# Kernel tuning notes

Hardware: AMD Instinct MI355X
Metric: run time of the kernel (lower is better)

The kernel has to match this reference:

```python
import jax, jax.numpy as jnp
import numpy as np

B, E, CIN, C, PRE, DME, DEN = 8, 64, 128, 128, 128, 32, 32
N_EDGE_TYPES, N_PATH_TYPES = 10, 20


def leaky(v):
    return jnp.where(v >= 0, v, 0.1 * v)


def setup_inputs() -> dict:
    key = jax.random.key(0)
    ks = jax.random.split(key, 30)
    s = 0.05
    inp = {
        'x': jax.random.normal(ks[0], (B, CIN, E), jnp.float32),
        'y': jax.random.normal(ks[1], (B, CIN, E), jnp.float32),
        'm_bias_mat': jax.random.normal(ks[2], (B, E, E), jnp.float32),
        'edge_mat': jax.random.randint(ks[3], (B, E, E), 0, N_EDGE_TYPES),
        'p_bias_mat': jax.random.normal(ks[4], (B, E, E, E), jnp.float32),
        'path_mat': jax.random.randint(ks[5], (B, E, E, E), 0, N_PATH_TYPES),
        'pre_out': jax.random.normal(ks[6], (B, PRE, E, E), jnp.float32),
        # parameters (conv1d/conv2d k=1 weights squeezed to matrices/vectors)
        'xc1_w': jax.random.normal(ks[7], (C, CIN), jnp.float32) * s,
        'yc1_w': jax.random.normal(ks[8], (C, CIN), jnp.float32) * s,
        'xc2_w': jax.random.normal(ks[9], (C,), jnp.float32) * s,
        'xc2_b': jax.random.normal(ks[10], (1,), jnp.float32) * s,
        'yc2_w': jax.random.normal(ks[11], (C,), jnp.float32) * s,
        'yc2_b': jax.random.normal(ks[12], (1,), jnp.float32) * s,
        'pconv_w': jax.random.normal(ks[13], (DEN,), jnp.float32) * s,
        'econv_w': jax.random.normal(ks[14], (DME,), jnp.float32) * s,
        'conv1_w': jax.random.normal(ks[15], (C, 2 * C + PRE), jnp.float32) * s,
        'conv1_b': jax.random.normal(ks[16], (C,), jnp.float32) * s,
        'conv2_w': jax.random.normal(ks[17], (C, C, 3, 3), jnp.float32) * s,
        'conv2_b': jax.random.normal(ks[18], (C,), jnp.float32) * s,
        'score_w': jax.random.normal(ks[19], (C,), jnp.float32) * s,
        'xlin_w': jax.random.normal(ks[20], (CIN, CIN), jnp.float32) * s,
        'ylin_w': jax.random.normal(ks[21], (CIN, CIN), jnp.float32) * s,
        'edge_table': jax.random.normal(ks[22], (N_EDGE_TYPES, DME), jnp.float32) * s,
        'path_table': jax.random.normal(ks[23], (N_PATH_TYPES, DEN), jnp.float32) * s,
    }
    return inp


def reference(x, y, m_bias_mat, edge_mat, p_bias_mat, path_mat, pre_out,
              xc1_w, yc1_w, xc2_w, xc2_b, yc2_w, yc2_b, pconv_w, econv_w,
              conv1_w, conv1_b, conv2_w, conv2_b, score_w, xlin_w, ylin_w,
              edge_table, path_table):
    # x,y: [B, CIN, E]; M == N == entity_num == E (required by path_fea reshape)
    x_f = jnp.einsum('ci,bim->bcm', xc1_w, x)                    # [B,C,M]
    y_f = jnp.einsum('ci,bin->bcn', yc1_w, y)                    # [B,C,N]
    x_self = jnp.einsum('c,bcm->bm', xc2_w, x_f) + xc2_b         # [B,M]
    y_other = jnp.einsum('c,bcn->bn', yc2_w, y_f) + yc2_b        # [B,N]
    # torch broadcast: [B,1,M] + [B,N,1] -> [B,N,M]
    logist = leaky(x_self[:, None, :] + y_other[:, :, None])     # [B,E,E]

    # ---- per-entity path attention (vectorized over entity axis e) ----
    path_embed = path_table[path_mat]                            # [B,E,M,N,DEN]
    path_logist = leaky(jnp.einsum('bemnd,d->bemn', path_embed, pconv_w))
    local = logist[:, None, :, :] + path_logist + p_bias_mat     # [B,E,M,N]
    A = jax.nn.softmax(local, axis=-1)
    x_ret = leaky(jnp.einsum('bemn,bcn->bcem', A, y_f) + x_f[:, :, None, :])  # [B,C,E,M]
    A2 = jax.nn.softmax(jnp.swapaxes(local, 2, 3), axis=-1)
    y_ret = leaky(jnp.einsum('benm,bcm->bcen', A2, x_f) + y_f[:, :, None, :])  # [B,C,E,N]
    path_fea = jnp.concatenate([x_ret, y_ret], axis=1)           # [B,2C,E,E]

    men = jnp.concatenate([path_fea, pre_out], axis=1)           # [B,2C+PRE,E,E]
    h = leaky(jnp.einsum('oc,bcij->boij', conv1_w, men) + conv1_b[None, :, None, None])
    h = jax.lax.conv_general_dilated(h, conv2_w, (1, 1), 'SAME',
                                     dimension_numbers=('NCHW', 'OIHW', 'NCHW'))
    men2rel = leaky(h + conv2_b[None, :, None, None])            # [B,C,E,E]

    scores = leaky(jnp.einsum('c,bcij->bij', score_w, men2rel))  # [B,E,E]
    edge_logist = leaky(jnp.einsum('bmnd,d->bmn', edge_table[edge_mat], econv_w))
    g = logist + scores + edge_logist + m_bias_mat               # [B,E,E]

    x_lin = jnp.einsum('ij,bjm->bmi', xlin_w, x)                 # [B,M,CIN]
    y_lin = jnp.einsum('ij,bjn->bni', ylin_w, y)                 # [B,N,CIN]
    G = jax.nn.softmax(g, axis=-1)
    out_x = jnp.einsum('bmn,bni->bim', G, y_lin) + x             # residual, [B,CIN,M]
    G2 = jax.nn.softmax(jnp.swapaxes(g, 1, 2), axis=-1)
    out_y = jnp.einsum('bnm,bmi->bin', G2, x_lin) + y            # [B,CIN,N]
    return (out_x, out_y, men2rel)
```

## Files before the change

kernel.cpp:

```cpp
#include <hip/hip_runtime.h>
#include <hip/hip_bf16.h>


typedef unsigned short u16;
typedef unsigned int u32;
typedef short s16x8 __attribute__((ext_vector_type(8)));
typedef float f32x4 __attribute__((ext_vector_type(4)));

#define NB 8
#define NE 64
#define NC 128

__device__ __forceinline__ float b2f(u16 u) { return __uint_as_float(((u32)u) << 16); }
__device__ __forceinline__ u16 f2b(float f) {
    u32 x = __float_as_uint(f);
    u32 r = (x + 0x7fffu + ((x >> 16) & 1u)) >> 16;
    return (u16)r;
}
__device__ __forceinline__ float lk(float v) { return v >= 0.f ? v : 0.1f * v; }
__device__ __forceinline__ s16x8 cvt8(const float* p) {
    float4 a = ((const float4*)p)[0], c = ((const float4*)p)[1];
    s16x8 r;
    r[0] = (short)f2b(a.x); r[1] = (short)f2b(a.y); r[2] = (short)f2b(a.z); r[3] = (short)f2b(a.w);
    r[4] = (short)f2b(c.x); r[5] = (short)f2b(c.y); r[6] = (short)f2b(c.z); r[7] = (short)f2b(c.w);
    return r;
}

__global__ __launch_bounds__(256) void k_prepw(const float* __restrict__ w1, const float* __restrict__ w2,
                                               u16* __restrict__ wA1, u16* __restrict__ wA2) {
    int idx = blockIdx.x * 256 + threadIdx.x;
    if (idx < 49152) {
        int e = idx & 7, lane = (idx >> 3) & 63, mtg = (idx >> 9) & 7, kc = idx >> 12;
        int o = mtg * 16 + (lane & 15), c = kc * 32 + ((lane >> 4) << 3) + e;
        wA1[idx] = f2b(w1[o * 384 + c]);
    } else {
        int id2 = idx - 49152;
        if (id2 < 147456) {
            int e = id2 & 7, lane = (id2 >> 3) & 63, mtg = (id2 >> 9) & 7;
            int kc = (id2 >> 12) & 3, tap = id2 >> 14;
            int o = mtg * 16 + (lane & 15), c = kc * 32 + ((lane >> 4) << 3) + e;
            wA2[id2] = f2b(w2[(o * 128 + c) * 9 + tap]);
        }
    }
}

__global__ __launch_bounds__(256) void k_front(const float* __restrict__ x, const float* __restrict__ y,
                                               const float* __restrict__ xc1, const float* __restrict__ yc1,
                                               const float* __restrict__ xc2w, const float* __restrict__ xc2b,
                                               const float* __restrict__ yc2w, const float* __restrict__ yc2b,
                                               const float* __restrict__ xlw, const float* __restrict__ ylw,
                                               const float* __restrict__ etab, const float* __restrict__ econv,
                                               const int* __restrict__ edge_mat, const float* __restrict__ m_bias,
                                               u16* __restrict__ xfb, u16* __restrict__ yfb,
                                               float* __restrict__ xfT, float* __restrict__ yfT,
                                               u16* __restrict__ xlT, u16* __restrict__ ylT,
                                               float* __restrict__ Lw, float* __restrict__ gb) {
    int b = blockIdx.x;
    int t = threadIdx.x;
    int lane = t & 63, w = t >> 6, l15 = lane & 15, q4 = lane >> 4;
    __shared__ u16 sxT[64][136];
    __shared__ u16 syT[64][136];
    __shared__ float sXs[64], sYo[64], sEd[16];

    if (t < 10) {
        float s = 0.f;
        for (int d = 0; d < 32; ++d) s += etab[t * 32 + d] * econv[d];
        sEd[t] = lk(s);
    }
    {
        int i = t >> 1, m0 = (t & 1) * 32;
        const float4* px = (const float4*)(x + (b * 128 + i) * 64 + m0);
        const float4* py = (const float4*)(y + (b * 128 + i) * 64 + m0);
#pragma unroll
        for (int q = 0; q < 8; ++q) {
            float4 v = px[q];
            int m = m0 + q * 4;
            sxT[m + 0][i] = f2b(v.x); sxT[m + 1][i] = f2b(v.y);
            sxT[m + 2][i] = f2b(v.z); sxT[m + 3][i] = f2b(v.w);
            float4 u = py[q];
            syT[m + 0][i] = f2b(u.x); syT[m + 1][i] = f2b(u.y);
            syT[m + 2][i] = f2b(u.z); syT[m + 3][i] = f2b(u.w);
        }
    }
    __syncthreads();

    int m = w * 16 + l15;

    {
        f32x4 acc[8];
#pragma unroll
        for (int mt = 0; mt < 8; ++mt) acc[mt] = (f32x4)(0.f);
#pragma unroll
        for (int kt = 0; kt < 4; ++kt) {
            s16x8 bfr = *(const s16x8*)&sxT[m][kt * 32 + q4 * 8];
#pragma unroll
            for (int mt = 0; mt < 8; ++mt) {
                s16x8 af = cvt8(xc1 + (mt * 16 + l15) * 128 + kt * 32 + q4 * 8);
                acc[mt] = __builtin_amdgcn_mfma_f32_16x16x32_bf16(af, bfr, acc[mt], 0, 0, 0);
            }
        }
        float xsp = 0.f;
#pragma unroll
        for (int mt = 0; mt < 8; ++mt) {
            int c0 = mt * 16 + q4 * 4;
            f32x4 a = acc[mt];
            xfb[(b * 128 + c0 + 0) * 64 + m] = f2b(a[0]);
            xfb[(b * 128 + c0 + 1) * 64 + m] = f2b(a[1]);
            xfb[(b * 128 + c0 + 2) * 64 + m] = f2b(a[2]);
            xfb[(b * 128 + c0 + 3) * 64 + m] = f2b(a[3]);
            *(float4*)(xfT + (b * 64 + m) * 128 + c0) = make_float4(a[0], a[1], a[2], a[3]);
            float4 wv = *(const float4*)(xc2w + c0);
            xsp += wv.x * a[0] + wv.y * a[1] + wv.z * a[2] + wv.w * a[3];
        }
        xsp += __shfl_xor(xsp, 16);
        xsp += __shfl_xor(xsp, 32);
        if (q4 == 0) sXs[m] = xsp + xc2b[0];
    }
    {
        f32x4 acc[8];
#pragma unroll
        for (int mt = 0; mt < 8; ++mt) acc[mt] = (f32x4)(0.f);
#pragma unroll
        for (int kt = 0; kt < 4; ++kt) {
            s16x8 bfr = *(const s16x8*)&syT[m][kt * 32 + q4 * 8];
#pragma unroll
            for (int mt = 0; mt < 8; ++mt) {
                s16x8 af = cvt8(yc1 + (mt * 16 + l15) * 128 + kt * 32 + q4 * 8);
                acc[mt] = __builtin_amdgcn_mfma_f32_16x16x32_bf16(af, bfr, acc[mt], 0, 0, 0);
            }
        }
        float ysp = 0.f;
#pragma unroll
        for (int mt = 0; mt < 8; ++mt) {
            int c0 = mt * 16 + q4 * 4;
            f32x4 a = acc[mt];
            yfb[(b * 128 + c0 + 0) * 64 + m] = f2b(a[0]);
            yfb[(b * 128 + c0 + 1) * 64 + m] = f2b(a[1]);
            yfb[(b * 128 + c0 + 2) * 64 + m] = f2b(a[2]);
            yfb[(b * 128 + c0 + 3) * 64 + m] = f2b(a[3]);
            *(float4*)(yfT + (b * 64 + m) * 128 + c0) = make_float4(a[0], a[1], a[2], a[3]);
            float4 wv = *(const float4*)(yc2w + c0);
            ysp += wv.x * a[0] + wv.y * a[1] + wv.z * a[2] + wv.w * a[3];
        }
        ysp += __shfl_xor(ysp, 16);
        ysp += __shfl_xor(ysp, 32);
        if (q4 == 0) sYo[m] = ysp + yc2b[0];
    }
    {
        f32x4 acc[8];
#pragma unroll
        for (int mt = 0; mt < 8; ++mt) acc[mt] = (f32x4)(0.f);
#pragma unroll
        for (int kt = 0; kt < 4; ++kt) {
            s16x8 bfr = *(const s16x8*)&sxT[m][kt * 32 + q4 * 8];
#pragma unroll
            for (int mt = 0; mt < 8; ++mt) {
                s16x8 af = cvt8(xlw + (mt * 16 + l15) * 128 + kt * 32 + q4 * 8);
                acc[mt] = __builtin_amdgcn_mfma_f32_16x16x32_bf16(af, bfr, acc[mt], 0, 0, 0);
            }
        }
#pragma unroll
        for (int mt = 0; mt < 8; ++mt) {
            int i0 = mt * 16 + q4 * 4;
            f32x4 a = acc[mt];
            xlT[(b * 128 + i0 + 0) * 64 + m] = f2b(a[0]);
            xlT[(b * 128 + i0 + 1) * 64 + m] = f2b(a[1]);
            xlT[(b * 128 + i0 + 2) * 64 + m] = f2b(a[2]);
            xlT[(b * 128 + i0 + 3) * 64 + m] = f2b(a[3]);
        }
    }
    {
        f32x4 acc[8];
#pragma unroll
        for (int mt = 0; mt < 8; ++mt) acc[mt] = (f32x4)(0.f);
#pragma unroll
        for (int kt = 0; kt < 4; ++kt) {
            s16x8 bfr = *(const s16x8*)&syT[m][kt * 32 + q4 * 8];
#pragma unroll
            for (int mt = 0; mt < 8; ++mt) {
                s16x8 af = cvt8(ylw + (mt * 16 + l15) * 128 + kt * 32 + q4 * 8);
                acc[mt] = __builtin_amdgcn_mfma_f32_16x16x32_bf16(af, bfr, acc[mt], 0, 0, 0);
            }
        }
#pragma unroll
        for (int mt = 0; mt < 8; ++mt) {
            int i0 = mt * 16 + q4 * 4;
            f32x4 a = acc[mt];
            ylT[(b * 128 + i0 + 0) * 64 + m] = f2b(a[0]);
            ylT[(b * 128 + i0 + 1) * 64 + m] = f2b(a[1]);
            ylT[(b * 128 + i0 + 2) * 64 + m] = f2b(a[2]);
            ylT[(b * 128 + i0 + 3) * 64 + m] = f2b(a[3]);
        }
    }
    __syncthreads();
#pragma unroll
    for (int r = 0; r < 16; ++r) {
        int idx = r * 256 + t;
        int i = idx >> 6, j = idx & 63;
        int gidx = b * 4096 + idx;
        float L = lk(sXs[j] + sYo[i]);
        Lw[gidx] = L;
        gb[gidx] = L + sEd[edge_mat[gidx]] + m_bias[gidx];
    }
}

__global__ __launch_bounds__(256) void k_attn(const float* __restrict__ Lw,
                                              const u16* __restrict__ xfb, const u16* __restrict__ yfb,
                                              const float* __restrict__ xfT, const float* __restrict__ yfT,
                                              const int* __restrict__ path_mat, const float* __restrict__ p_bias,
                                              const float* __restrict__ ptab, const float* __restrict__ pconv,
                                              const float* __restrict__ pre, u16* __restrict__ menT) {
    int b = blockIdx.x >> 6, e = blockIdx.x & 63;
    int t = threadIdx.x;
    int lane = t & 63, w = t >> 6;
    __shared__ float sA[64][68];
    __shared__ u16 Abf[64][72];
    __shared__ u16 E2bf[64][72];
    __shared__ float sRed[256];
    __shared__ float sPdot[20];

    if (t < 20) {
        float s = 0.f;
        for (int d = 0; d < 32; ++d) s += ptab[t * 32 + d] * pconv[d];
        sPdot[t] = lk(s);
    }
    __syncthreads();

    {
        int m = t >> 2, n0 = (t & 3) * 16;
        int base = (((b * 64 + e) * 64 + m) * 64 + n0);
        const int4* pm4 = (const int4*)(path_mat + base);
        const float4* pb4 = (const float4*)(p_bias + base);
        const float4* L4 = (const float4*)(Lw + (b * 64 + m) * 64 + n0);
#pragma unroll
        for (int q = 0; q < 4; ++q) {
            int4 pm = pm4[q]; float4 pb = pb4[q]; float4 l = L4[q];
            float4 v;
            v.x = l.x + sPdot[pm.x] + pb.x;
            v.y = l.y + sPdot[pm.y] + pb.y;
            v.z = l.z + sPdot[pm.z] + pb.z;
            v.w = l.w + sPdot[pm.w] + pb.w;
            *(float4*)&sA[m][n0 + q * 4] = v;
        }
    }
    __syncthreads();

    if (t < 128) {
        int r = t >> 1, h = t & 1;
        const float4* rp = (const float4*)&sA[r][h * 32];
        float mx = -1e30f;
#pragma unroll
        for (int k = 0; k < 8; ++k) {
            float4 v = rp[k];
            mx = fmaxf(mx, fmaxf(fmaxf(v.x, v.y), fmaxf(v.z, v.w)));
        }
        mx = fmaxf(mx, __shfl_xor(mx, 1));
        float s = 0.f;
#pragma unroll
        for (int k = 0; k < 8; ++k) {
            float4 v = rp[k];
            s += __expf(v.x - mx) + __expf(v.y - mx) + __expf(v.z - mx) + __expf(v.w - mx);
        }
        s += __shfl_xor(s, 1);
        if (h == 0) { sRed[r] = mx; sRed[64 + r] = 1.f / s; }
    } else {
        int n = (t - 128) >> 1, h = t & 1;
        float mx = -1e30f;
#pragma unroll
        for (int k = 0; k < 32; ++k) mx = fmaxf(mx, sA[h * 32 + k][n]);
        mx = fmaxf(mx, __shfl_xor(mx, 1));
        float s = 0.f;
#pragma unroll
        for (int k = 0; k < 32; ++k) s += __expf(sA[h * 32 + k][n] - mx);
        s += __shfl_xor(s, 1);
        if (h == 0) { sRed[128 + n] = mx; sRed[192 + n] = 1.f / s; }
    }
    __syncthreads();

    {
        int m = t >> 2, q = t & 3;
        float rmax = sRed[m], rinv = sRed[64 + m];
        const float4* rp = (const float4*)&sA[m][q * 16];
#pragma unroll
        for (int g2 = 0; g2 < 2; ++g2) {
            float4 v0 = rp[g2 * 2], v1 = rp[g2 * 2 + 1];
            s16x8 pk;
            pk[0] = (short)f2b(__expf(v0.x - rmax) * rinv);
            pk[1] = (short)f2b(__expf(v0.y - rmax) * rinv);
            pk[2] = (short)f2b(__expf(v0.z - rmax) * rinv);
            pk[3] = (short)f2b(__expf(v0.w - rmax) * rinv);
            pk[4] = (short)f2b(__expf(v1.x - rmax) * rinv);
            pk[5] = (short)f2b(__expf(v1.y - rmax) * rinv);
            pk[6] = (short)f2b(__expf(v1.z - rmax) * rinv);
            pk[7] = (short)f2b(__expf(v1.w - rmax) * rinv);
            *(s16x8*)&Abf[m][q * 16 + g2 * 8] = pk;
        }
    }
    {
        int n = t >> 2, q = t & 3;
        float cmax = sRed[128 + n], cinv = sRed[192 + n];
#pragma unroll
        for (int g2 = 0; g2 < 2; ++g2) {
            s16x8 pk;
#pragma unroll
            for (int k = 0; k < 8; ++k) {
                float v = sA[q * 16 + g2 * 8 + k][n];
                pk[k] = (short)f2b(__expf(v - cmax) * cinv);
            }
            *(s16x8*)&E2bf[n][q * 16 + g2 * 8] = pk;
        }
    }
    __syncthreads();

    int l15 = lane & 15, q4 = lane >> 4;
    {
        f32x4 acc[2][4];
#pragma unroll
        for (int ci = 0; ci < 2; ++ci)
#pragma unroll
            for (int mt = 0; mt < 4; ++mt) acc[ci][mt] = (f32x4)(0.f);
#pragma unroll
        for (int kt = 0; kt < 2; ++kt) {
            s16x8 afr[2];
#pragma unroll
            for (int ci = 0; ci < 2; ++ci) {
                int c = (2 * w + ci) * 16 + l15;
                afr[ci] = *(const s16x8*)(yfb + (b * 128 + c) * 64 + kt * 32 + q4 * 8);
            }
            s16x8 bfr[4];
#pragma unroll
            for (int mt = 0; mt < 4; ++mt)
                bfr[mt] = *(const s16x8*)&Abf[mt * 16 + l15][kt * 32 + q4 * 8];
#pragma unroll
            for (int ci = 0; ci < 2; ++ci)
#pragma unroll
                for (int mt = 0; mt < 4; ++mt)
                    acc[ci][mt] = __builtin_amdgcn_mfma_f32_16x16x32_bf16(afr[ci], bfr[mt], acc[ci][mt], 0, 0, 0);
        }
#pragma unroll
        for (int ci = 0; ci < 2; ++ci) {
            int c0 = (2 * w + ci) * 16 + q4 * 4;
#pragma unroll
            for (int mt = 0; mt < 4; ++mt) {
                int m = mt * 16 + l15;
                float4 res = *(const float4*)(xfT + (b * 64 + m) * 128 + c0);
                f32x4 a = acc[ci][mt];
                u32 lo = (u32)f2b(lk(a[0] + res.x)) | ((u32)f2b(lk(a[1] + res.y)) << 16);
                u32 hi = (u32)f2b(lk(a[2] + res.z)) | ((u32)f2b(lk(a[3] + res.w)) << 16);
                *(uint2*)(menT + ((b * 64 + e) * 64 + m) * 384 + c0) = make_uint2(lo, hi);
            }
        }
    }
    {
        f32x4 acc[2][4];
#pragma unroll
        for (int ci = 0; ci < 2; ++ci)
#pragma unroll
            for (int nt = 0; nt < 4; ++nt) acc[ci][nt] = (f32x4)(0.f);
#pragma unroll
        for (int kt = 0; kt < 2; ++kt) {
            s16x8 afr[2];
#pragma unroll
            for (int ci = 0; ci < 2; ++ci) {
                int c = (2 * w + ci) * 16 + l15;
                afr[ci] = *(const s16x8*)(xfb + (b * 128 + c) * 64 + kt * 32 + q4 * 8);
            }
            s16x8 bfr[4];
#pragma unroll
            for (int nt = 0; nt < 4; ++nt)
                bfr[nt] = *(const s16x8*)&E2bf[nt * 16 + l15][kt * 32 + q4 * 8];
#pragma unroll
            for (int ci = 0; ci < 2; ++ci)
#pragma unroll
                for (int nt = 0; nt < 4; ++nt)
                    acc[ci][nt] = __builtin_amdgcn_mfma_f32_16x16x32_bf16(afr[ci], bfr[nt], acc[ci][nt], 0, 0, 0);
        }
#pragma unroll
        for (int ci = 0; ci < 2; ++ci) {
            int c0 = (2 * w + ci) * 16 + q4 * 4;
#pragma unroll
            for (int nt = 0; nt < 4; ++nt) {
                int n = nt * 16 + l15;
                float4 res = *(const float4*)(yfT + (b * 64 + n) * 128 + c0);
                f32x4 a = acc[ci][nt];
                u32 lo = (u32)f2b(lk(a[0] + res.x)) | ((u32)f2b(lk(a[1] + res.y)) << 16);
                u32 hi = (u32)f2b(lk(a[2] + res.z)) | ((u32)f2b(lk(a[3] + res.w)) << 16);
                *(uint2*)(menT + ((b * 64 + e) * 64 + n) * 384 + 128 + c0) = make_uint2(lo, hi);
            }
        }
    }
    {
        int j = t & 63, pg = t >> 6;
#pragma unroll
        for (int oc = 0; oc < 4; ++oc) {
            int p0 = pg * 32 + oc * 8;
            s16x8 v;
#pragma unroll
            for (int k = 0; k < 8; ++k)
                v[k] = (short)f2b(pre[((b * 128 + p0 + k) * 64 + e) * 64 + j]);
            *(s16x8*)(menT + ((b * 64 + e) * 64 + j) * 384 + 256 + p0) = v;
        }
    }
}

__global__ __launch_bounds__(256) void k_conv1(const u16* __restrict__ menT, const u16* __restrict__ wA1,
                                               const float* __restrict__ b1, u16* __restrict__ hT) {
    int b = blockIdx.x >> 6, i = blockIdx.x & 63;
    int t = threadIdx.x;
    int lane = t & 63, w = t >> 6, wm = w & 1, wn = w >> 1;
    int l15 = lane & 15, q4 = lane >> 4;

    f32x4 acc[4][2];
#pragma unroll
    for (int mt = 0; mt < 4; ++mt)
#pragma unroll
        for (int nt = 0; nt < 2; ++nt) acc[mt][nt] = (f32x4)(0.f);

    const u16* mrow = menT + (b * 64 + i) * 64 * 384;
    for (int kc = 0; kc < 12; ++kc) {
        s16x8 af[4];
#pragma unroll
        for (int mt = 0; mt < 4; ++mt)
            af[mt] = *(const s16x8*)(wA1 + (((kc * 8 + wm * 4 + mt) * 64 + lane) << 3));
        s16x8 bf[2];
#pragma unroll
        for (int nt = 0; nt < 2; ++nt) {
            int j = (wn * 2 + nt) * 16 + l15;
            bf[nt] = *(const s16x8*)(mrow + j * 384 + kc * 32 + q4 * 8);
        }
#pragma unroll
        for (int mt = 0; mt < 4; ++mt)
#pragma unroll
            for (int nt = 0; nt < 2; ++nt)
                acc[mt][nt] = __builtin_amdgcn_mfma_f32_16x16x32_bf16(af[mt], bf[nt], acc[mt][nt], 0, 0, 0);
    }

#pragma unroll
    for (int mt = 0; mt < 4; ++mt) {
        int o0 = (wm * 4 + mt) * 16 + q4 * 4;
        float4 bb = *(const float4*)(b1 + o0);
#pragma unroll
        for (int nt = 0; nt < 2; ++nt) {
            int j = (wn * 2 + nt) * 16 + l15;
            f32x4 a = acc[mt][nt];
            u32 lo = (u32)f2b(lk(a[0] + bb.x)) | ((u32)f2b(lk(a[1] + bb.y)) << 16);
            u32 hi = (u32)f2b(lk(a[2] + bb.z)) | ((u32)f2b(lk(a[3] + bb.w)) << 16);
            *(uint2*)(hT + ((b * 64 + i) * 64 + j) * 128 + o0) = make_uint2(lo, hi);
        }
    }
}

__global__ __launch_bounds__(256) void k_conv2(const u16* __restrict__ hT, const u16* __restrict__ wA2,
                                               const float* __restrict__ b2, const float* __restrict__ score_w,
                                               const float* __restrict__ gb, float* __restrict__ m2r,
                                               float* __restrict__ g) {
    int b = blockIdx.x >> 6, i = blockIdx.x & 63;
    int t = threadIdx.x;
    int lane = t & 63, w = t >> 6, wm = w & 1, wn = w >> 1;
    int l15 = lane & 15, q4 = lane >> 4;
    __shared__ u16 sB2[3][66][136];
    __shared__ float sSc[2][64];

#pragma unroll
    for (int q = 0; q < 2; ++q) {
        int u = q * 256 + t;
        if (u < 384) {
            int r = u >> 7, rem = u & 127, hcol = rem >> 6, c2 = rem & 63;
            *(u32*)&sB2[r][hcol ? 65 : 0][c2 * 2] = 0u;
        }
    }
#pragma unroll
    for (int it = 0; it < 12; ++it) {
        int u = it * 256 + t;
        int cg = u & 15, j = (u >> 4) & 63, r = u >> 10;
        int ir = i - 1 + r;
        int4 v = make_int4(0, 0, 0, 0);
        if (ir >= 0 && ir < 64)
            v = *(const int4*)(hT + ((b * 64 + ir) * 64 + j) * 128 + cg * 8);
        *(int4*)&sB2[r][j + 1][cg * 8] = v;
    }
    __syncthreads();

    f32x4 acc[4][2];
#pragma unroll
    for (int mt = 0; mt < 4; ++mt)
#pragma unroll
        for (int nt = 0; nt < 2; ++nt) acc[mt][nt] = (f32x4)(0.f);

    for (int kc = 0; kc < 4; ++kc) {
#pragma unroll
        for (int tap = 0; tap < 9; ++tap) {
            int di = tap / 3, dj = tap % 3;
            s16x8 af[4];
#pragma unroll
            for (int mt = 0; mt < 4; ++mt)
                af[mt] = *(const s16x8*)(wA2 + ((((tap * 4 + kc) * 8 + wm * 4 + mt) * 64 + lane) << 3));
#pragma unroll
            for (int nt = 0; nt < 2; ++nt) {
                int jin = wn * 32 + nt * 16 + l15 + dj;
                s16x8 bf = *(const s16x8*)(&sB2[di][jin][kc * 32 + q4 * 8]);
#pragma unroll
                for (int mt = 0; mt < 4; ++mt)
                    acc[mt][nt] = __builtin_amdgcn_mfma_f32_16x16x32_bf16(af[mt], bf, acc[mt][nt], 0, 0, 0);
            }
        }
    }

    float part[2] = {0.f, 0.f};
#pragma unroll
    for (int mt = 0; mt < 4; ++mt) {
        int o0 = wm * 64 + mt * 16 + q4 * 4;
        float4 bb = *(const float4*)(b2 + o0);
        float4 sw = *(const float4*)(score_w + o0);
#pragma unroll
        for (int nt = 0; nt < 2; ++nt) {
            int j = wn * 32 + nt * 16 + l15;
            f32x4 a = acc[mt][nt];
            float v0 = lk(a[0] + bb.x), v1 = lk(a[1] + bb.y);
            float v2 = lk(a[2] + bb.z), v3 = lk(a[3] + bb.w);
            float* dst = m2r + ((b * 128 + o0) * 64 + i) * 64 + j;
            dst[0] = v0; dst[4096] = v1; dst[8192] = v2; dst[12288] = v3;
            part[nt] += sw.x * v0 + sw.y * v1 + sw.z * v2 + sw.w * v3;
        }
    }
#pragma unroll
    for (int nt = 0; nt < 2; ++nt) {
        float p = part[nt];
        p += __shfl_xor(p, 16);
        p += __shfl_xor(p, 32);
        if (q4 == 0) sSc[wm][wn * 32 + nt * 16 + l15] = p;
    }
    __syncthreads();
    if (t < 64) {
        float s = sSc[0][t] + sSc[1][t];
        int gi = (b * 64 + i) * 64 + t;
        g[gi] = gb[gi] + lk(s);
    }
}

__global__ __launch_bounds__(256) void k_gout(const float* __restrict__ g,
                                              const u16* __restrict__ xlT, const u16* __restrict__ ylT,
                                              const float* __restrict__ x, const float* __restrict__ y,
                                              float* __restrict__ out) {
    int b = blockIdx.x;
    int t = threadIdx.x;
    int lane = t & 63, w = t >> 6, l15 = lane & 15, q4 = lane >> 4;
    __shared__ float sG[64][68];
    __shared__ u16 Gbf[64][72];
    __shared__ u16 G2bf[64][72];
    __shared__ float sRed[256];

#pragma unroll
    for (int r = 0; r < 16; ++r) {
        int idx = r * 256 + t;
        sG[idx >> 6][idx & 63] = g[b * 4096 + idx];
    }
    __syncthreads();

    if (t < 128) {
        int r = t >> 1, h = t & 1;
        const float4* rp = (const float4*)&sG[r][h * 32];
        float mx = -1e30f;
#pragma unroll
        for (int k = 0; k < 8; ++k) {
            float4 v = rp[k];
            mx = fmaxf(mx, fmaxf(fmaxf(v.x, v.y), fmaxf(v.z, v.w)));
        }
        mx = fmaxf(mx, __shfl_xor(mx, 1));
        float s = 0.f;
#pragma unroll
        for (int k = 0; k < 8; ++k) {
            float4 v = rp[k];
            s += __expf(v.x - mx) + __expf(v.y - mx) + __expf(v.z - mx) + __expf(v.w - mx);
        }
        s += __shfl_xor(s, 1);
        if (h == 0) { sRed[r] = mx; sRed[64 + r] = 1.f / s; }
    } else {
        int n = (t - 128) >> 1, h = t & 1;
        float mx = -1e30f;
#pragma unroll
        for (int k = 0; k < 32; ++k) mx = fmaxf(mx, sG[h * 32 + k][n]);
        mx = fmaxf(mx, __shfl_xor(mx, 1));
        float s = 0.f;
#pragma unroll
        for (int k = 0; k < 32; ++k) s += __expf(sG[h * 32 + k][n] - mx);
        s += __shfl_xor(s, 1);
        if (h == 0) { sRed[128 + n] = mx; sRed[192 + n] = 1.f / s; }
    }
    __syncthreads();

    {
        int m = t >> 2, q = t & 3;
        float rmax = sRed[m], rinv = sRed[64 + m];
        const float4* rp = (const float4*)&sG[m][q * 16];
#pragma unroll
        for (int g2 = 0; g2 < 2; ++g2) {
            float4 v0 = rp[g2 * 2], v1 = rp[g2 * 2 + 1];
            s16x8 pk;
            pk[0] = (short)f2b(__expf(v0.x - rmax) * rinv);
            pk[1] = (short)f2b(__expf(v0.y - rmax) * rinv);
            pk[2] = (short)f2b(__expf(v0.z - rmax) * rinv);
            pk[3] = (short)f2b(__expf(v0.w - rmax) * rinv);
            pk[4] = (short)f2b(__expf(v1.x - rmax) * rinv);
            pk[5] = (short)f2b(__expf(v1.y - rmax) * rinv);
            pk[6] = (short)f2b(__expf(v1.z - rmax) * rinv);
            pk[7] = (short)f2b(__expf(v1.w - rmax) * rinv);
            *(s16x8*)&Gbf[m][q * 16 + g2 * 8] = pk;
        }
    }
    {
        int n = t >> 2, q = t & 3;
        float cmax = sRed[128 + n], cinv = sRed[192 + n];
#pragma unroll
        for (int g2 = 0; g2 < 2; ++g2) {
            s16x8 pk;
#pragma unroll
            for (int k = 0; k < 8; ++k) {
                float v = sG[q * 16 + g2 * 8 + k][n];
                pk[k] = (short)f2b(__expf(v - cmax) * cinv);
            }
            *(s16x8*)&G2bf[n][q * 16 + g2 * 8] = pk;
        }
    }
    __syncthreads();

    int mcol = w * 16 + l15;
    {
        f32x4 acc[8];
#pragma unroll
        for (int mt = 0; mt < 8; ++mt) acc[mt] = (f32x4)(0.f);
#pragma unroll
        for (int kt = 0; kt < 2; ++kt) {
            s16x8 bfr = *(const s16x8*)&Gbf[mcol][kt * 32 + q4 * 8];
#pragma unroll
            for (int mt = 0; mt < 8; ++mt) {
                s16x8 af = *(const s16x8*)(ylT + (b * 128 + mt * 16 + l15) * 64 + kt * 32 + q4 * 8);
                acc[mt] = __builtin_amdgcn_mfma_f32_16x16x32_bf16(af, bfr, acc[mt], 0, 0, 0);
            }
        }
#pragma unroll
        for (int mt = 0; mt < 8; ++mt) {
            int i0 = mt * 16 + q4 * 4;
            f32x4 a = acc[mt];
#pragma unroll
            for (int r = 0; r < 4; ++r) {
                int ad = (b * 128 + i0 + r) * 64 + mcol;
                out[ad] = a[r] + x[ad];
            }
        }
    }
    {
        f32x4 acc[8];
#pragma unroll
        for (int mt = 0; mt < 8; ++mt) acc[mt] = (f32x4)(0.f);
#pragma unroll
        for (int kt = 0; kt < 2; ++kt) {
            s16x8 bfr = *(const s16x8*)&G2bf[mcol][kt * 32 + q4 * 8];
#pragma unroll
            for (int mt = 0; mt < 8; ++mt) {
                s16x8 af = *(const s16x8*)(xlT + (b * 128 + mt * 16 + l15) * 64 + kt * 32 + q4 * 8);
                acc[mt] = __builtin_amdgcn_mfma_f32_16x16x32_bf16(af, bfr, acc[mt], 0, 0, 0);
            }
        }
#pragma unroll
        for (int mt = 0; mt < 8; ++mt) {
            int i0 = mt * 16 + q4 * 4;
            f32x4 a = acc[mt];
#pragma unroll
            for (int r = 0; r < 4; ++r) {
                int ad = (b * 128 + i0 + r) * 64 + mcol;
                out[65536 + ad] = a[r] + y[ad];
            }
        }
    }
}

extern "C" void kernel_launch(void* const* d_in, const int* in_sizes, int n_in,
                              void* d_out, int out_size, void* d_ws, size_t ws_size,
                              hipStream_t stream) {
    const float* x = (const float*)d_in[0];
    const float* y = (const float*)d_in[1];
    const float* m_bias = (const float*)d_in[2];
    const int* edge_mat = (const int*)d_in[3];
    const float* p_bias = (const float*)d_in[4];
    const int* path_mat = (const int*)d_in[5];
    const float* pre = (const float*)d_in[6];
    const float* xc1 = (const float*)d_in[7];
    const float* yc1 = (const float*)d_in[8];
    const float* xc2w = (const float*)d_in[9];
    const float* xc2b = (const float*)d_in[10];
    const float* yc2w = (const float*)d_in[11];
    const float* yc2b = (const float*)d_in[12];
    const float* pconv = (const float*)d_in[13];
    const float* econv = (const float*)d_in[14];
    const float* w1 = (const float*)d_in[15];
    const float* b1 = (const float*)d_in[16];
    const float* w2 = (const float*)d_in[17];
    const float* b2 = (const float*)d_in[18];
    const float* score_w = (const float*)d_in[19];
    const float* xlw = (const float*)d_in[20];
    const float* ylw = (const float*)d_in[21];
    const float* etab = (const float*)d_in[22];
    const float* ptab = (const float*)d_in[23];

    float* Lw = (float*)d_ws;
    float* gb = Lw + 32768;
    float* g = gb + 32768;
    float* xfT = g + 32768;
    float* yfT = xfT + 65536;
    u16* wA1 = (u16*)(yfT + 65536);
    u16* wA2 = wA1 + 49152;
    u16* xfb = wA2 + 147456;
    u16* yfb = xfb + 65536;
    u16* xlT = yfb + 65536;
    u16* ylT = xlT + 65536;
    u16* menT = ylT + 65536;
    u16* hT = menT + 12582912;

    float* out = (float*)d_out;
    float* out_m2r = out + 131072;

    hipLaunchKernelGGL(k_prepw, dim3(768), dim3(256), 0, stream, w1, w2, wA1, wA2);
    hipLaunchKernelGGL(k_front, dim3(8), dim3(256), 0, stream, x, y, xc1, yc1, xc2w, xc2b,
                       yc2w, yc2b, xlw, ylw, etab, econv, edge_mat, m_bias,
                       xfb, yfb, xfT, yfT, xlT, ylT, Lw, gb);
    hipLaunchKernelGGL(k_attn, dim3(512), dim3(256), 0, stream, Lw, xfb, yfb, xfT, yfT,
                       path_mat, p_bias, ptab, pconv, pre, menT);
    hipLaunchKernelGGL(k_conv1, dim3(512), dim3(256), 0, stream, menT, wA1, b1, hT);
    hipLaunchKernelGGL(k_conv2, dim3(512), dim3(256), 0, stream, hT, wA2, b2, score_w, gb,
                       out_m2r, g);
    hipLaunchKernelGGL(k_gout, dim3(8), dim3(256), 0, stream, g, xlT, ylT, x, y, out);
}
```

Measured before the change: 219.0 us.

## Merge weight prep and front projections into one wide kernel, split gout by direction

The weight-reformat kernel and the 8-block front kernel are combined into a single launch. The four projection GEMMs now run in separate blocks (32 instead of 8), and the pre_out-to-menT transpose moves out of k_attn into extra blocks of the same launch. The leaky logit matrix and the gb buffer are no longer stored; they are recomputed from per-node Xs/Yo vectors inside k_attn and k_conv2. The output kernel splits the row and column softmax paths across twice as many blocks. The aim is to remove a serial low-parallelism stage and a launch, at the cost of some recomputation and a larger mixed-role grid.

```diff
diff --git a/kernel.cpp b/kernel.cpp
--- a/kernel.cpp
+++ b/kernel.cpp
@@ -6,10 +6,6 @@
 typedef unsigned int u32;
 typedef short s16x8 __attribute__((ext_vector_type(8)));
 typedef float f32x4 __attribute__((ext_vector_type(4)));
-
-#define NB 8
-#define NE 64
-#define NC 128
 
 __device__ __forceinline__ float b2f(u16 u) { return __uint_as_float(((u32)u) << 16); }
 __device__ __forceinline__ u16 f2b(float f) {
@@ -26,190 +22,127 @@
     return r;
 }
 
-__global__ __launch_bounds__(256) void k_prepw(const float* __restrict__ w1, const float* __restrict__ w2,
-                                               u16* __restrict__ wA1, u16* __restrict__ wA2) {
-    int idx = blockIdx.x * 256 + threadIdx.x;
-    if (idx < 49152) {
-        int e = idx & 7, lane = (idx >> 3) & 63, mtg = (idx >> 9) & 7, kc = idx >> 12;
-        int o = mtg * 16 + (lane & 15), c = kc * 32 + ((lane >> 4) << 3) + e;
-        wA1[idx] = f2b(w1[o * 384 + c]);
-    } else {
-        int id2 = idx - 49152;
-        if (id2 < 147456) {
-            int e = id2 & 7, lane = (id2 >> 3) & 63, mtg = (id2 >> 9) & 7;
-            int kc = (id2 >> 12) & 3, tap = id2 >> 14;
+__global__ __launch_bounds__(256) void k_prep(const float* __restrict__ w1, const float* __restrict__ w2,
+                                              u16* __restrict__ wA1, u16* __restrict__ wA2,
+                                              const float* __restrict__ x, const float* __restrict__ y,
+                                              const float* __restrict__ xc1, const float* __restrict__ yc1,
+                                              const float* __restrict__ xc2w, const float* __restrict__ xc2b,
+                                              const float* __restrict__ yc2w, const float* __restrict__ yc2b,
+                                              const float* __restrict__ xlw, const float* __restrict__ ylw,
+                                              u16* __restrict__ xfb, u16* __restrict__ yfb,
+                                              float* __restrict__ xfT, float* __restrict__ yfT,
+                                              u16* __restrict__ xlT, u16* __restrict__ ylT,
+                                              float* __restrict__ Xs, float* __restrict__ Yo,
+                                              const float* __restrict__ pre, u16* __restrict__ menT) {
+    int bid = blockIdx.x;
+    int t = threadIdx.x;
+    if (bid < 768) {
+        int idx = bid * 256 + t;
+        if (idx < 49152) {
+            int e = idx & 7, lane = (idx >> 3) & 63, mtg = (idx >> 9) & 7, kc = idx >> 12;
             int o = mtg * 16 + (lane & 15), c = kc * 32 + ((lane >> 4) << 3) + e;
-            wA2[id2] = f2b(w2[(o * 128 + c) * 9 + tap]);
-        }
-    }
-}
-
-__global__ __launch_bounds__(256) void k_front(const float* __restrict__ x, const float* __restrict__ y,
-                                               const float* __restrict__ xc1, const float* __restrict__ yc1,
-                                               const float* __restrict__ xc2w, const float* __restrict__ xc2b,
-                                               const float* __restrict__ yc2w, const float* __restrict__ yc2b,
-                                               const float* __restrict__ xlw, const float* __restrict__ ylw,
-                                               const float* __restrict__ etab, const float* __restrict__ econv,
-                                               const int* __restrict__ edge_mat, const float* __restrict__ m_bias,
-                                               u16* __restrict__ xfb, u16* __restrict__ yfb,
-                                               float* __restrict__ xfT, float* __restrict__ yfT,
-                                               u16* __restrict__ xlT, u16* __restrict__ ylT,
-                                               float* __restrict__ Lw, float* __restrict__ gb) {
-    int b = blockIdx.x;
-    int t = threadIdx.x;
-    int lane = t & 63, w = t >> 6, l15 = lane & 15, q4 = lane >> 4;
-    __shared__ u16 sxT[64][136];
-    __shared__ u16 syT[64][136];
-    __shared__ float sXs[64], sYo[64], sEd[16];
-
-    if (t < 10) {
-        float s = 0.f;
-        for (int d = 0; d < 32; ++d) s += etab[t * 32 + d] * econv[d];
-        sEd[t] = lk(s);
+            wA1[idx] = f2b(w1[o * 384 + c]);
+        } else {
+            int id2 = idx - 49152;
+            if (id2 < 147456) {
+                int e = id2 & 7, lane = (id2 >> 3) & 63, mtg = (id2 >> 9) & 7;
+                int kc = (id2 >> 12) & 3, tap = id2 >> 14;
+                int o = mtg * 16 + (lane & 15), c = kc * 32 + ((lane >> 4) << 3) + e;
+                wA2[id2] = f2b(w2[(o * 128 + c) * 9 + tap]);
+            }
+        }
+        return;
+    }
+    if (bid < 800) {
+        int r = bid - 768;
+        int b = r >> 2, g4 = r & 3;
+        int lane = t & 63, w = t >> 6, l15 = lane & 15, q4 = lane >> 4;
+        __shared__ u16 sT[64][136];
+        const float* src = (g4 == 0 || g4 == 2) ? x : y;
+        const float* wptr = (g4 == 0) ? xc1 : (g4 == 1) ? yc1 : (g4 == 2) ? xlw : ylw;
+        {
+            int i = t >> 1, m0 = (t & 1) * 32;
+            const float4* ps = (const float4*)(src + (b * 128 + i) * 64 + m0);
+#pragma unroll
+            for (int q = 0; q < 8; ++q) {
+                float4 v = ps[q];
+                int m = m0 + q * 4;
+                sT[m + 0][i] = f2b(v.x); sT[m + 1][i] = f2b(v.y);
+                sT[m + 2][i] = f2b(v.z); sT[m + 3][i] = f2b(v.w);
+            }
+        }
+        __syncthreads();
+        int m = w * 16 + l15;
+        f32x4 acc[8];
+#pragma unroll
+        for (int mt = 0; mt < 8; ++mt) acc[mt] = (f32x4)(0.f);
+#pragma unroll
+        for (int kt = 0; kt < 4; ++kt) {
+            s16x8 bfr = *(const s16x8*)&sT[m][kt * 32 + q4 * 8];
+#pragma unroll
+            for (int mt = 0; mt < 8; ++mt) {
+                s16x8 af = cvt8(wptr + (mt * 16 + l15) * 128 + kt * 32 + q4 * 8);
+                acc[mt] = __builtin_amdgcn_mfma_f32_16x16x32_bf16(af, bfr, acc[mt], 0, 0, 0);
+            }
+        }
+        if (g4 == 0 || g4 == 1) {
+            u16* fb = (g4 == 0) ? xfb : yfb;
+            float* fT = (g4 == 0) ? xfT : yfT;
+            const float* c2w = (g4 == 0) ? xc2w : yc2w;
+            const float* c2b = (g4 == 0) ? xc2b : yc2b;
+            float* dvec = (g4 == 0) ? Xs : Yo;
+            float sp = 0.f;
+#pragma unroll
+            for (int mt = 0; mt < 8; ++mt) {
+                int c0 = mt * 16 + q4 * 4;
+                f32x4 a = acc[mt];
+                fb[(b * 128 + c0 + 0) * 64 + m] = f2b(a[0]);
+                fb[(b * 128 + c0 + 1) * 64 + m] = f2b(a[1]);
+                fb[(b * 128 + c0 + 2) * 64 + m] = f2b(a[2]);
+                fb[(b * 128 + c0 + 3) * 64 + m] = f2b(a[3]);
+                *(float4*)(fT + (b * 64 + m) * 128 + c0) = make_float4(a[0], a[1], a[2], a[3]);
+                float4 wv = *(const float4*)(c2w + c0);
+                sp += wv.x * a[0] + wv.y * a[1] + wv.z * a[2] + wv.w * a[3];
+            }
+            sp += __shfl_xor(sp, 16);
+            sp += __shfl_xor(sp, 32);
+            if (q4 == 0) dvec[b * 64 + m] = sp + c2b[0];
+        } else {
+            u16* lT = (g4 == 2) ? xlT : ylT;
+#pragma unroll
+            for (int mt = 0; mt < 8; ++mt) {
+                int i0 = mt * 16 + q4 * 4;
+                f32x4 a = acc[mt];
+                lT[(b * 128 + i0 + 0) * 64 + m] = f2b(a[0]);
+                lT[(b * 128 + i0 + 1) * 64 + m] = f2b(a[1]);
+                lT[(b * 128 + i0 + 2) * 64 + m] = f2b(a[2]);
+                lT[(b * 128 + i0 + 3) * 64 + m] = f2b(a[3]);
+            }
+        }
+        return;
     }
     {
-        int i = t >> 1, m0 = (t & 1) * 32;
-        const float4* px = (const float4*)(x + (b * 128 + i) * 64 + m0);
-        const float4* py = (const float4*)(y + (b * 128 + i) * 64 + m0);
-#pragma unroll
-        for (int q = 0; q < 8; ++q) {
-            float4 v = px[q];
-            int m = m0 + q * 4;
-            sxT[m + 0][i] = f2b(v.x); sxT[m + 1][i] = f2b(v.y);
-            sxT[m + 2][i] = f2b(v.z); sxT[m + 3][i] = f2b(v.w);
-            float4 u = py[q];
-            syT[m + 0][i] = f2b(u.x); syT[m + 1][i] = f2b(u.y);
-            syT[m + 2][i] = f2b(u.z); syT[m + 3][i] = f2b(u.w);
-        }
-    }
-    __syncthreads();
-
-    int m = w * 16 + l15;
-
-    {
-        f32x4 acc[8];
-#pragma unroll
-        for (int mt = 0; mt < 8; ++mt) acc[mt] = (f32x4)(0.f);
-#pragma unroll
-        for (int kt = 0; kt < 4; ++kt) {
-            s16x8 bfr = *(const s16x8*)&sxT[m][kt * 32 + q4 * 8];
-#pragma unroll
-            for (int mt = 0; mt < 8; ++mt) {
-                s16x8 af = cvt8(xc1 + (mt * 16 + l15) * 128 + kt * 32 + q4 * 8);
-                acc[mt] = __builtin_amdgcn_mfma_f32_16x16x32_bf16(af, bfr, acc[mt], 0, 0, 0);
-            }
-        }
-        float xsp = 0.f;
-#pragma unroll
-        for (int mt = 0; mt < 8; ++mt) {
-            int c0 = mt * 16 + q4 * 4;
-            f32x4 a = acc[mt];
-            xfb[(b * 128 + c0 + 0) * 64 + m] = f2b(a[0]);
-            xfb[(b * 128 + c0 + 1) * 64 + m] = f2b(a[1]);
-            xfb[(b * 128 + c0 + 2) * 64 + m] = f2b(a[2]);
-            xfb[(b * 128 + c0 + 3) * 64 + m] = f2b(a[3]);
-            *(float4*)(xfT + (b * 64 + m) * 128 + c0) = make_float4(a[0], a[1], a[2], a[3]);
-            float4 wv = *(const float4*)(xc2w + c0);
-            xsp += wv.x * a[0] + wv.y * a[1] + wv.z * a[2] + wv.w * a[3];
-        }
-        xsp += __shfl_xor(xsp, 16);
-        xsp += __shfl_xor(xsp, 32);
-        if (q4 == 0) sXs[m] = xsp + xc2b[0];
-    }
-    {
-        f32x4 acc[8];
-#pragma unroll
-        for (int mt = 0; mt < 8; ++mt) acc[mt] = (f32x4)(0.f);
-#pragma unroll
-        for (int kt = 0; kt < 4; ++kt) {
-            s16x8 bfr = *(const s16x8*)&syT[m][kt * 32 + q4 * 8];
-#pragma unroll
-            for (int mt = 0; mt < 8; ++mt) {
-                s16x8 af = cvt8(yc1 + (mt * 16 + l15) * 128 + kt * 32 + q4 * 8);
-                acc[mt] = __builtin_amdgcn_mfma_f32_16x16x32_bf16(af, bfr, acc[mt], 0, 0, 0);
-            }
-        }
-        float ysp = 0.f;
-#pragma unroll
-        for (int mt = 0; mt < 8; ++mt) {
-            int c0 = mt * 16 + q4 * 4;
-            f32x4 a = acc[mt];
-            yfb[(b * 128 + c0 + 0) * 64 + m] = f2b(a[0]);
-            yfb[(b * 128 + c0 + 1) * 64 + m] = f2b(a[1]);
-            yfb[(b * 128 + c0 + 2) * 64 + m] = f2b(a[2]);
-            yfb[(b * 128 + c0 + 3) * 64 + m] = f2b(a[3]);
-            *(float4*)(yfT + (b * 64 + m) * 128 + c0) = make_float4(a[0], a[1], a[2], a[3]);
-            float4 wv = *(const float4*)(yc2w + c0);
-            ysp += wv.x * a[0] + wv.y * a[1] + wv.z * a[2] + wv.w * a[3];
-        }
-        ysp += __shfl_xor(ysp, 16);
-        ysp += __shfl_xor(ysp, 32);
-        if (q4 == 0) sYo[m] = ysp + yc2b[0];
-    }
-    {
-        f32x4 acc[8];
-#pragma unroll
-        for (int mt = 0; mt < 8; ++mt) acc[mt] = (f32x4)(0.f);
-#pragma unroll
-        for (int kt = 0; kt < 4; ++kt) {
-            s16x8 bfr = *(const s16x8*)&sxT[m][kt * 32 + q4 * 8];
-#pragma unroll
-            for (int mt = 0; mt < 8; ++mt) {
-                s16x8 af = cvt8(xlw + (mt * 16 + l15) * 128 + kt * 32 + q4 * 8);
-                acc[mt] = __builtin_amdgcn_mfma_f32_16x16x32_bf16(af, bfr, acc[mt], 0, 0, 0);
-            }
-        }
-#pragma unroll
-        for (int mt = 0; mt < 8; ++mt) {
-            int i0 = mt * 16 + q4 * 4;
-            f32x4 a = acc[mt];
-            xlT[(b * 128 + i0 + 0) * 64 + m] = f2b(a[0]);
-            xlT[(b * 128 + i0 + 1) * 64 + m] = f2b(a[1]);
-            xlT[(b * 128 + i0 + 2) * 64 + m] = f2b(a[2]);
-            xlT[(b * 128 + i0 + 3) * 64 + m] = f2b(a[3]);
-        }
-    }
-    {
-        f32x4 acc[8];
-#pragma unroll
-        for (int mt = 0; mt < 8; ++mt) acc[mt] = (f32x4)(0.f);
-#pragma unroll
-        for (int kt = 0; kt < 4; ++kt) {
-            s16x8 bfr = *(const s16x8*)&syT[m][kt * 32 + q4 * 8];
-#pragma unroll
-            for (int mt = 0; mt < 8; ++mt) {
-                s16x8 af = cvt8(ylw + (mt * 16 + l15) * 128 + kt * 32 + q4 * 8);
-                acc[mt] = __builtin_amdgcn_mfma_f32_16x16x32_bf16(af, bfr, acc[mt], 0, 0, 0);
-            }
-        }
-#pragma unroll
-        for (int mt = 0; mt < 8; ++mt) {
-            int i0 = mt * 16 + q4 * 4;
-            f32x4 a = acc[mt];
-            ylT[(b * 128 + i0 + 0) * 64 + m] = f2b(a[0]);
-            ylT[(b * 128 + i0 + 1) * 64 + m] = f2b(a[1]);
-            ylT[(b * 128 + i0 + 2) * 64 + m] = f2b(a[2]);
-            ylT[(b * 128 + i0 + 3) * 64 + m] = f2b(a[3]);
-        }
-    }
-    __syncthreads();
-#pragma unroll
-    for (int r = 0; r < 16; ++r) {
-        int idx = r * 256 + t;
-        int i = idx >> 6, j = idx & 63;
-        int gidx = b * 4096 + idx;
-        float L = lk(sXs[j] + sYo[i]);
-        Lw[gidx] = L;
-        gb[gidx] = L + sEd[edge_mat[gidx]] + m_bias[gidx];
-    }
-}
-
-__global__ __launch_bounds__(256) void k_attn(const float* __restrict__ Lw,
+        int r = bid - 800;
+        int b = r >> 6, i = r & 63;
+        int j = t & 63, pg = t >> 6;
+#pragma unroll
+        for (int oc = 0; oc < 4; ++oc) {
+            int p0 = pg * 32 + oc * 8;
+            s16x8 v;
+#pragma unroll
+            for (int k = 0; k < 8; ++k)
+                v[k] = (short)f2b(pre[((b * 128 + p0 + k) * 64 + i) * 64 + j]);
+            *(s16x8*)(menT + ((b * 64 + i) * 64 + j) * 384 + 256 + p0) = v;
+        }
+    }
+}
+
+__global__ __launch_bounds__(256) void k_attn(const float* __restrict__ Xs, const float* __restrict__ Yo,
                                               const u16* __restrict__ xfb, const u16* __restrict__ yfb,
                                               const float* __restrict__ xfT, const float* __restrict__ yfT,
                                               const int* __restrict__ path_mat, const float* __restrict__ p_bias,
                                               const float* __restrict__ ptab, const float* __restrict__ pconv,
-                                              const float* __restrict__ pre, u16* __restrict__ menT) {
+                                              u16* __restrict__ menT) {
     int b = blockIdx.x >> 6, e = blockIdx.x & 63;
     int t = threadIdx.x;
     int lane = t & 63, w = t >> 6;
@@ -218,11 +151,16 @@
     __shared__ u16 E2bf[64][72];
     __shared__ float sRed[256];
     __shared__ float sPdot[20];
+    __shared__ float sXv[64], sYv[64];
 
     if (t < 20) {
         float s = 0.f;
         for (int d = 0; d < 32; ++d) s += ptab[t * 32 + d] * pconv[d];
         sPdot[t] = lk(s);
+    } else if (t >= 64 && t < 128) {
+        sXv[t - 64] = Xs[b * 64 + t - 64];
+    } else if (t >= 128 && t < 192) {
+        sYv[t - 128] = Yo[b * 64 + t - 128];
     }
     __syncthreads();
 
@@ -231,16 +169,17 @@
         int base = (((b * 64 + e) * 64 + m) * 64 + n0);
         const int4* pm4 = (const int4*)(path_mat + base);
         const float4* pb4 = (const float4*)(p_bias + base);
-        const float4* L4 = (const float4*)(Lw + (b * 64 + m) * 64 + n0);
+        float yom = sYv[m];
 #pragma unroll
         for (int q = 0; q < 4; ++q) {
-            int4 pm = pm4[q]; float4 pb = pb4[q]; float4 l = L4[q];
+            int4 pm = pm4[q]; float4 pb = pb4[q];
+            int n = n0 + q * 4;
             float4 v;
-            v.x = l.x + sPdot[pm.x] + pb.x;
-            v.y = l.y + sPdot[pm.y] + pb.y;
-            v.z = l.z + sPdot[pm.z] + pb.z;
-            v.w = l.w + sPdot[pm.w] + pb.w;
-            *(float4*)&sA[m][n0 + q * 4] = v;
+            v.x = lk(sXv[n + 0] + yom) + sPdot[pm.x] + pb.x;
+            v.y = lk(sXv[n + 1] + yom) + sPdot[pm.y] + pb.y;
+            v.z = lk(sXv[n + 2] + yom) + sPdot[pm.z] + pb.z;
+            v.w = lk(sXv[n + 3] + yom) + sPdot[pm.w] + pb.w;
+            *(float4*)&sA[m][n] = v;
         }
     }
     __syncthreads();
@@ -389,18 +328,6 @@
             }
         }
     }
-    {
-        int j = t & 63, pg = t >> 6;
-#pragma unroll
-        for (int oc = 0; oc < 4; ++oc) {
-            int p0 = pg * 32 + oc * 8;
-            s16x8 v;
-#pragma unroll
-            for (int k = 0; k < 8; ++k)
-                v[k] = (short)f2b(pre[((b * 128 + p0 + k) * 64 + e) * 64 + j]);
-            *(s16x8*)(menT + ((b * 64 + e) * 64 + j) * 384 + 256 + p0) = v;
-        }
-    }
 }
 
 __global__ __launch_bounds__(256) void k_conv1(const u16* __restrict__ menT, const u16* __restrict__ wA1,
@@ -452,15 +379,24 @@
 
 __global__ __launch_bounds__(256) void k_conv2(const u16* __restrict__ hT, const u16* __restrict__ wA2,
                                                const float* __restrict__ b2, const float* __restrict__ score_w,
-                                               const float* __restrict__ gb, float* __restrict__ m2r,
-                                               float* __restrict__ g) {
+                                               const float* __restrict__ Xs, const float* __restrict__ Yo,
+                                               const float* __restrict__ etab, const float* __restrict__ econv,
+                                               const int* __restrict__ edge_mat, const float* __restrict__ m_bias,
+                                               float* __restrict__ m2r, float* __restrict__ g) {
     int b = blockIdx.x >> 6, i = blockIdx.x & 63;
     int t = threadIdx.x;
     int lane = t & 63, w = t >> 6, wm = w & 1, wn = w >> 1;
     int l15 = lane & 15, q4 = lane >> 4;
     __shared__ u16 sB2[3][66][136];
     __shared__ float sSc[2][64];
-
+    __shared__ float sEd[16];
+
+    if (t >= 240 && t < 250) {
+        int et = t - 240;
+        float s = 0.f;
+        for (int d = 0; d < 32; ++d) s += etab[et * 32 + d] * econv[d];
+        sEd[et] = lk(s);
+    }
 #pragma unroll
     for (int q = 0; q < 2; ++q) {
         int u = q * 256 + t;
@@ -534,7 +470,8 @@
     if (t < 64) {
         float s = sSc[0][t] + sSc[1][t];
         int gi = (b * 64 + i) * 64 + t;
-        g[gi] = gb[gi] + lk(s);
+        float L = lk(Xs[b * 64 + t] + Yo[b * 64 + i]);
+        g[gi] = L + sEd[edge_mat[gi]] + m_bias[gi] + lk(s);
     }
 }
 
@@ -542,13 +479,12 @@
                                               const u16* __restrict__ xlT, const u16* __restrict__ ylT,
                                               const float* __restrict__ x, const float* __restrict__ y,
                                               float* __restrict__ out) {
-    int b = blockIdx.x;
+    int b = blockIdx.x >> 1, which = blockIdx.x & 1;
     int t = threadIdx.x;
     int lane = t & 63, w = t >> 6, l15 = lane & 15, q4 = lane >> 4;
     __shared__ float sG[64][68];
     __shared__ u16 Gbf[64][72];
-    __shared__ u16 G2bf[64][72];
-    __shared__ float sRed[256];
+    __shared__ float sRed[128];
 
 #pragma unroll
     for (int r = 0; r < 16; ++r) {
@@ -557,39 +493,27 @@
     }
     __syncthreads();
 
-    if (t < 128) {
-        int r = t >> 1, h = t & 1;
-        const float4* rp = (const float4*)&sG[r][h * 32];
-        float mx = -1e30f;
-#pragma unroll
-        for (int k = 0; k < 8; ++k) {
-            float4 v = rp[k];
-            mx = fmaxf(mx, fmaxf(fmaxf(v.x, v.y), fmaxf(v.z, v.w)));
-        }
-        mx = fmaxf(mx, __shfl_xor(mx, 1));
-        float s = 0.f;
-#pragma unroll
-        for (int k = 0; k < 8; ++k) {
-            float4 v = rp[k];
-            s += __expf(v.x - mx) + __expf(v.y - mx) + __expf(v.z - mx) + __expf(v.w - mx);
-        }
-        s += __shfl_xor(s, 1);
-        if (h == 0) { sRed[r] = mx; sRed[64 + r] = 1.f / s; }
-    } else {
-        int n = (t - 128) >> 1, h = t & 1;
-        float mx = -1e30f;
-#pragma unroll
-        for (int k = 0; k < 32; ++k) mx = fmaxf(mx, sG[h * 32 + k][n]);
-        mx = fmaxf(mx, __shfl_xor(mx, 1));
-        float s = 0.f;
-#pragma unroll
-        for (int k = 0; k < 32; ++k) s += __expf(sG[h * 32 + k][n] - mx);
-        s += __shfl_xor(s, 1);
-        if (h == 0) { sRed[128 + n] = mx; sRed[192 + n] = 1.f / s; }
-    }
-    __syncthreads();
-
-    {
+    if (which == 0) {
+        if (t < 128) {
+            int r = t >> 1, h = t & 1;
+            const float4* rp = (const float4*)&sG[r][h * 32];
+            float mx = -1e30f;
+#pragma unroll
+            for (int k = 0; k < 8; ++k) {
+                float4 v = rp[k];
+                mx = fmaxf(mx, fmaxf(fmaxf(v.x, v.y), fmaxf(v.z, v.w)));
+            }
+            mx = fmaxf(mx, __shfl_xor(mx, 1));
+            float s = 0.f;
+#pragma unroll
+            for (int k = 0; k < 8; ++k) {
+                float4 v = rp[k];
+                s += __expf(v.x - mx) + __expf(v.y - mx) + __expf(v.z - mx) + __expf(v.w - mx);
+            }
+            s += __shfl_xor(s, 1);
+            if (h == 0) { sRed[r] = mx; sRed[64 + r] = 1.f / s; }
+        }
+        __syncthreads();
         int m = t >> 2, q = t & 3;
         float rmax = sRed[m], rinv = sRed[64 + m];
         const float4* rp = (const float4*)&sG[m][q * 16];
@@ -607,10 +531,22 @@
             pk[7] = (short)f2b(__expf(v1.w - rmax) * rinv);
             *(s16x8*)&Gbf[m][q * 16 + g2 * 8] = pk;
         }
-    }
-    {
+    } else {
+        if (t < 128) {
+            int n = t >> 1, h = t & 1;
+            float mx = -1e30f;
+#pragma unroll
+            for (int k = 0; k < 32; ++k) mx = fmaxf(mx, sG[h * 32 + k][n]);
+            mx = fmaxf(mx, __shfl_xor(mx, 1));
+            float s = 0.f;
+#pragma unroll
+            for (int k = 0; k < 32; ++k) s += __expf(sG[h * 32 + k][n] - mx);
+            s += __shfl_xor(s, 1);
+            if (h == 0) { sRed[n] = mx; sRed[64 + n] = 1.f / s; }
+        }
+        __syncthreads();
         int n = t >> 2, q = t & 3;
-        float cmax = sRed[128 + n], cinv = sRed[192 + n];
+        float cmax = sRed[n], cinv = sRed[64 + n];
 #pragma unroll
         for (int g2 = 0; g2 < 2; ++g2) {
             s16x8 pk;
@@ -619,58 +555,35 @@
                 float v = sG[q * 16 + g2 * 8 + k][n];
                 pk[k] = (short)f2b(__expf(v - cmax) * cinv);
             }
-            *(s16x8*)&G2bf[n][q * 16 + g2 * 8] = pk;
-        }
-    }
-    __syncthreads();
-
+            *(s16x8*)&Gbf[n][q * 16 + g2 * 8] = pk;
+        }
+    }
+    __syncthreads();
+
+    const u16* lT = which ? xlT : ylT;
+    const float* res = which ? y : x;
+    int off = which ? 65536 : 0;
     int mcol = w * 16 + l15;
-    {
-        f32x4 acc[8];
-#pragma unroll
-        for (int mt = 0; mt < 8; ++mt) acc[mt] = (f32x4)(0.f);
-#pragma unroll
-        for (int kt = 0; kt < 2; ++kt) {
-            s16x8 bfr = *(const s16x8*)&Gbf[mcol][kt * 32 + q4 * 8];
-#pragma unroll
-            for (int mt = 0; mt < 8; ++mt) {
-                s16x8 af = *(const s16x8*)(ylT + (b * 128 + mt * 16 + l15) * 64 + kt * 32 + q4 * 8);
-                acc[mt] = __builtin_amdgcn_mfma_f32_16x16x32_bf16(af, bfr, acc[mt], 0, 0, 0);
-            }
-        }
+    f32x4 acc[8];
+#pragma unroll
+    for (int mt = 0; mt < 8; ++mt) acc[mt] = (f32x4)(0.f);
+#pragma unroll
+    for (int kt = 0; kt < 2; ++kt) {
+        s16x8 bfr = *(const s16x8*)&Gbf[mcol][kt * 32 + q4 * 8];
 #pragma unroll
         for (int mt = 0; mt < 8; ++mt) {
-            int i0 = mt * 16 + q4 * 4;
-            f32x4 a = acc[mt];
-#pragma unroll
-            for (int r = 0; r < 4; ++r) {
-                int ad = (b * 128 + i0 + r) * 64 + mcol;
-                out[ad] = a[r] + x[ad];
-            }
-        }
-    }
-    {
-        f32x4 acc[8];
-#pragma unroll
-        for (int mt = 0; mt < 8; ++mt) acc[mt] = (f32x4)(0.f);
-#pragma unroll
-        for (int kt = 0; kt < 2; ++kt) {
-            s16x8 bfr = *(const s16x8*)&G2bf[mcol][kt * 32 + q4 * 8];
-#pragma unroll
-            for (int mt = 0; mt < 8; ++mt) {
-                s16x8 af = *(const s16x8*)(xlT + (b * 128 + mt * 16 + l15) * 64 + kt * 32 + q4 * 8);
-                acc[mt] = __builtin_amdgcn_mfma_f32_16x16x32_bf16(af, bfr, acc[mt], 0, 0, 0);
-            }
-        }
-#pragma unroll
-        for (int mt = 0; mt < 8; ++mt) {
-            int i0 = mt * 16 + q4 * 4;
-            f32x4 a = acc[mt];
-#pragma unroll
-            for (int r = 0; r < 4; ++r) {
-                int ad = (b * 128 + i0 + r) * 64 + mcol;
-                out[65536 + ad] = a[r] + y[ad];
-            }
+            s16x8 af = *(const s16x8*)(lT + (b * 128 + mt * 16 + l15) * 64 + kt * 32 + q4 * 8);
+            acc[mt] = __builtin_amdgcn_mfma_f32_16x16x32_bf16(af, bfr, acc[mt], 0, 0, 0);
+        }
+    }
+#pragma unroll
+    for (int mt = 0; mt < 8; ++mt) {
+        int i0 = mt * 16 + q4 * 4;
+        f32x4 a = acc[mt];
+#pragma unroll
+        for (int r = 0; r < 4; ++r) {
+            int ad = (b * 128 + i0 + r) * 64 + mcol;
+            out[off + ad] = a[r] + res[ad];
         }
     }
 }
@@ -703,9 +616,9 @@
     const float* etab = (const float*)d_in[22];
     const float* ptab = (const float*)d_in[23];
 
-    float* Lw = (float*)d_ws;
-    float* gb = Lw + 32768;
-    float* g = gb + 32768;
+    float* Xs = (float*)d_ws;
+    float* Yo = Xs + 512;
+    float* g = Yo + 512;
     float* xfT = g + 32768;
     float* yfT = xfT + 65536;
     u16* wA1 = (u16*)(yfT + 65536);
@@ -720,14 +633,13 @@
     float* out = (float*)d_out;
     float* out_m2r = out + 131072;
 
-    hipLaunchKernelGGL(k_prepw, dim3(768), dim3(256), 0, stream, w1, w2, wA1, wA2);
-    hipLaunchKernelGGL(k_front, dim3(8), dim3(256), 0, stream, x, y, xc1, yc1, xc2w, xc2b,
-                       yc2w, yc2b, xlw, ylw, etab, econv, edge_mat, m_bias,
-                       xfb, yfb, xfT, yfT, xlT, ylT, Lw, gb);
-    hipLaunchKernelGGL(k_attn, dim3(512), dim3(256), 0, stream, Lw, xfb, yfb, xfT, yfT,
-                       path_mat, p_bias, ptab, pconv, pre, menT);
+    hipLaunchKernelGGL(k_prep, dim3(1312), dim3(256), 0, stream, w1, w2, wA1, wA2,
+                       x, y, xc1, yc1, xc2w, xc2b, yc2w, yc2b, xlw, ylw,
+                       xfb, yfb, xfT, yfT, xlT, ylT, Xs, Yo, pre, menT);
+    hipLaunchKernelGGL(k_attn, dim3(512), dim3(256), 0, stream, Xs, Yo, xfb, yfb, xfT, yfT,
+                       path_mat, p_bias, ptab, pconv, menT);
     hipLaunchKernelGGL(k_conv1, dim3(512), dim3(256), 0, stream, menT, wA1, b1, hT);
-    hipLaunchKernelGGL(k_conv2, dim3(512), dim3(256), 0, stream, hT, wA2, b2, score_w, gb,
-                       out_m2r, g);
-    hipLaunchKernelGGL(k_gout, dim3(8), dim3(256), 0, stream, g, xlT, ylT, x, y, out);
-}
+    hipLaunchKernelGGL(k_conv2, dim3(512), dim3(256), 0, stream, hT, wA2, b2, score_w,
+                       Xs, Yo, etab, econv, edge_mat, m_bias, out_m2r, g);
+    hipLaunchKernelGGL(k_gout, dim3(16), dim3(256), 0, stream, g, xlT, ylT, x, y, out);
+}
```

Result: faster. 190.5 us (-13.0%).
